# Optimization experiments

Hardware: AMD Instinct MI355X
Metric: run time of the kernel (lower is better)

## Reference

```python
import jax, jax.numpy as jnp
import numpy as np

B, LF, RATE = 2, 2048, 4
DF, DS, H = 1024, 1024, 8
D2 = DF // 2            # 512: both self (d1) and cross (d2) branch dims (equal split)
POOL_H = 2048
TS = LF // RATE         # 512 slow steps


def _p(key, shape):
    return jax.random.normal(key, shape, jnp.float32) * 0.02


def setup_inputs() -> dict:
    keys = iter(jax.random.split(jax.random.key(0), 32))
    inp = {
        "x_fast": jax.random.normal(next(keys), (B, LF, DF), jnp.float32),
        "x_slow": jax.random.normal(next(keys), (B, TS, DS), jnp.float32),
    }
    for name in ("fself", "fcross", "sself", "scross"):
        inp[f"{name}_wqkv"] = _p(next(keys), (D2, 3 * D2))
        inp[f"{name}_bqkv"] = jnp.zeros((3 * D2,), jnp.float32)
        inp[f"{name}_wo"] = _p(next(keys), (D2, D2))
        inp[f"{name}_bo"] = jnp.zeros((D2,), jnp.float32)
    inp["lift_w"] = _p(next(keys), (DS, D2))
    inp["lift_b"] = jnp.zeros((D2,), jnp.float32)
    inp["pool_w1"] = _p(next(keys), (RATE * DF, POOL_H))
    inp["pool_b1"] = jnp.zeros((POOL_H,), jnp.float32)
    inp["pool_w2"] = _p(next(keys), (POOL_H, D2))
    inp["pool_b2"] = jnp.zeros((D2,), jnp.float32)
    return inp


def _mha(q_in, k_in, v_in, wqkv, bqkv, wo, bo):
    """Standard multihead attention with fused in-proj weight [d, 3d]."""
    b, tq, d = q_in.shape
    hd = d // H
    q = q_in @ wqkv[:, :d] + bqkv[:d]
    k = k_in @ wqkv[:, d:2 * d] + bqkv[d:2 * d]
    v = v_in @ wqkv[:, 2 * d:] + bqkv[2 * d:]
    q = q.reshape(b, tq, H, hd)
    k = k.reshape(b, k_in.shape[1], H, hd)
    v = v.reshape(b, v_in.shape[1], H, hd)
    scores = jnp.einsum('bqhd,bkhd->bhqk', q, k) * np.float32(1.0 / np.sqrt(hd))
    w = jax.nn.softmax(scores, axis=-1)
    o = jnp.einsum('bhqk,bkhd->bqhd', w, v).reshape(b, tq, d)
    return o @ wo + bo


def _forward(x_fast, x_slow,
             fself_wqkv, fself_bqkv, fself_wo, fself_bo,
             fcross_wqkv, fcross_bqkv, fcross_wo, fcross_bo,
             sself_wqkv, sself_bqkv, sself_wo, sself_bo,
             scross_wqkv, scross_bqkv, scross_wo, scross_bo,
             lift_w, lift_b, pool_w1, pool_b1, pool_w2, pool_b2):
    b = x_fast.shape[0]
    # ---- fast level: lift slow -> fast timescale (ffn applied before repeat)
    y = jnp.repeat(x_slow @ lift_w + lift_b, RATE, axis=1)          # [B, LF, D2]
    x1, x2 = x_fast[..., :D2], x_fast[..., D2:]
    z_fast = jnp.concatenate([
        _mha(x1, x1, x1, fself_wqkv, fself_bqkv, fself_wo, fself_bo),
        _mha(x2, y, y, fcross_wqkv, fcross_bqkv, fcross_wo, fcross_bo),
    ], axis=-1)
    # ---- slow level: causal block pooling of fast sequence
    blocks = x_fast.reshape(b, TS, RATE * DF)                        # LF == TS*RATE
    s = jax.nn.gelu(blocks @ pool_w1 + pool_b1) @ pool_w2 + pool_b2  # [B, TS, D2]
    # causal shift: prepend zero slow step, drop last (zero in pooled feature dim)
    s = jnp.concatenate([jnp.zeros((b, 1, D2), s.dtype), s[:, :-1]], axis=1)
    s1, s2 = x_slow[..., :D2], x_slow[..., D2:]
    z_slow = jnp.concatenate([
        _mha(s1, s1, s1, sself_wqkv, sself_bqkv, sself_wo, sself_bo),
        _mha(s2, s, s, scross_wqkv, scross_bqkv, scross_wo, scross_bo),
    ], axis=-1)
    return z_fast, z_slow


def reference(x_fast, x_slow,
              fself_wqkv, fself_bqkv, fself_wo, fself_bo,
              fcross_wqkv, fcross_bqkv, fcross_wo, fcross_bo,
              sself_wqkv, sself_bqkv, sself_wo, sself_bo,
              scross_wqkv, scross_bqkv, scross_wo, scross_bo,
              lift_w, lift_b, pool_w1, pool_b1, pool_w2, pool_b2):
    return _forward(x_fast, x_slow,
                    fself_wqkv, fself_bqkv, fself_wo, fself_bo,
                    fcross_wqkv, fcross_bqkv, fcross_wo, fcross_bo,
                    sself_wqkv, sself_bqkv, sself_wo, sself_bo,
                    scross_wqkv, scross_bqkv, scross_wo, scross_bo,
                    lift_w, lift_b, pool_w1, pool_b1, pool_w2, pool_b2)
```

## Files before the change

kernel.cpp:

```cpp
#include <hip/hip_runtime.h>
#include <hip/hip_bf16.h>


typedef __attribute__((ext_vector_type(8))) short bf16x8;
typedef __attribute__((ext_vector_type(4))) float f32x4;
typedef unsigned short u16;
typedef unsigned int u32;

__device__ inline u16 f2bf(float f) {
    __hip_bfloat16 h = __float2bfloat16(f);
    return *reinterpret_cast<u16*>(&h);
}
__device__ inline u32 pack2(float a, float b) {
    return (u32)f2bf(a) | ((u32)f2bf(b) << 16);
}
__device__ inline float bf2f(u16 h) {
    u32 x = ((u32)h) << 16; float f;
    __builtin_memcpy(&f, &x, 4);
    return f;
}

#define LDT 72

struct GDesc {
    const void* A; const u16* Bt; const float* bias;
    void* out0; u16* aux0; u16* aux1;
    int lda, ldb, ldc, K, ntx, mode, rshift, aflag, tile_end, pad;
};
struct GPack { int n; int pad[3]; GDesc d[8]; };

template <int TMT>
__global__ __launch_bounds__(256)
void gemm_multi(GPack pk)
{
    constexpr int TM = TMT * 16;
    constexpr int W = TMT / 2;
    __shared__ u16 As[TM * LDT];
    __shared__ u16 Bs[TM * LDT];

    int bid = blockIdx.x;
    int di = 0;
    while (bid >= pk.d[di].tile_end) ++di;
    const GDesc g = pk.d[di];
    const int base = di ? pk.d[di - 1].tile_end : 0;
    const int local = bid - base;
    const int ty = local / g.ntx, tx = local - ty * g.ntx;
    const int row0 = ty * TM, col0 = tx * TM;

    const int t = threadIdx.x;
    const int wave = t >> 6, lane = t & 63;
    const int l15 = lane & 15, quad = lane >> 4;
    const int wm = (wave >> 1) * W * 16, wn = (wave & 1) * W * 16;
    const int sr = t >> 3, sc = t & 7;

    f32x4 acc[W][W];
#pragma unroll
    for (int i = 0; i < W; ++i)
#pragma unroll
        for (int j = 0; j < W; ++j) {
            acc[i][j][0] = 0.f; acc[i][j][1] = 0.f;
            acc[i][j][2] = 0.f; acc[i][j][3] = 0.f;
        }

    for (int k0 = 0; k0 < g.K; k0 += 64) {
        __syncthreads();
        if (g.aflag) {
            const float* Af = (const float*)g.A;
#pragma unroll
            for (int i = 0; i < TM / 32; ++i) {
                int r = sr + 32 * i;
                const float* p = Af + (long long)(row0 + r) * g.lda + k0 + sc * 8;
                float4 a = *(const float4*)p;
                float4 b = *(const float4*)(p + 4);
                uint4 u;
                u.x = pack2(a.x, a.y); u.y = pack2(a.z, a.w);
                u.z = pack2(b.x, b.y); u.w = pack2(b.z, b.w);
                *(uint4*)(As + r * LDT + sc * 8) = u;
            }
        } else {
            const u16* Ab = (const u16*)g.A;
#pragma unroll
            for (int i = 0; i < TM / 32; ++i) {
                int r = sr + 32 * i;
                *(uint4*)(As + r * LDT + sc * 8) =
                    *(const uint4*)(Ab + (long long)(row0 + r) * g.lda + k0 + sc * 8);
            }
        }
#pragma unroll
        for (int i = 0; i < TM / 32; ++i) {
            int r = sr + 32 * i;
            *(uint4*)(Bs + r * LDT + sc * 8) =
                *(const uint4*)(g.Bt + (long long)(col0 + r) * g.ldb + k0 + sc * 8);
        }
        __syncthreads();
#pragma unroll
        for (int kc = 0; kc < 2; ++kc) {
            bf16x8 af[W], bfr[W];
#pragma unroll
            for (int i = 0; i < W; ++i) {
                af[i]  = *(const bf16x8*)(As + (wm + i * 16 + l15) * LDT + kc * 32 + quad * 8);
                bfr[i] = *(const bf16x8*)(Bs + (wn + i * 16 + l15) * LDT + kc * 32 + quad * 8);
            }
#pragma unroll
            for (int i = 0; i < W; ++i)
#pragma unroll
                for (int j = 0; j < W; ++j)
                    acc[i][j] = __builtin_amdgcn_mfma_f32_16x16x32_bf16(af[i], bfr[j], acc[i][j], 0, 0, 0);
        }
    }

    const int rmask = (1 << g.rshift) - 1;
#pragma unroll
    for (int i = 0; i < W; ++i)
#pragma unroll
        for (int j = 0; j < W; ++j)
#pragma unroll
            for (int r = 0; r < 4; ++r) {
                int m = row0 + wm + i * 16 + quad * 4 + r;
                int n = col0 + wn + j * 16 + l15;
                float v = acc[i][j][r];
                if (g.mode != 5) v += g.bias[n];
                if (g.mode == 0) {
                    ((float*)g.out0)[(long long)m * g.ldc + n] = v;
                } else if (g.mode == 1 || g.mode == 5) {
                    ((u16*)g.out0)[(long long)m * g.ldc + n] = f2bf(v);
                } else if (g.mode == 3) {
                    u16 h = f2bf(v);
                    if (n < 512) ((u16*)g.out0)[(long long)m * 512 + n] = h;
                    else if (n < 1024) g.aux0[(long long)m * 512 + (n - 512)] = h;
                    else {
                        int d = n - 1024;
                        int bb = m >> g.rshift, rr = m & rmask;
                        g.aux1[((long long)((bb * 8 + (d >> 6)) * 64 + (d & 63)) << g.rshift) + rr] = h;
                    }
                } else if (g.mode == 4) {
                    u16 h = f2bf(v);
                    if (n < 512) ((u16*)g.out0)[(long long)m * 512 + n] = h;
                    else {
                        int d = n - 512;
                        int bb = m >> g.rshift, rr = m & rmask;
                        g.aux1[((long long)((bb * 8 + (d >> 6)) * 64 + (d & 63)) << g.rshift) + rr] = h;
                    }
                } else {
                    int t9 = m & 511;
                    if (t9 != 511) ((u16*)g.out0)[(long long)(m + 1) * g.ldc + n] = f2bf(v);
                    if (t9 == 0)  ((u16*)g.out0)[(long long)m * g.ldc + n] = 0;
                }
            }
}

#define ALD 72

struct ADesc { const u16* Q; const u16* K; const u16* Vt; u16* O; int Rq, nk, tile_end, pad; };
struct APack { int n; int pad[3]; ADesc d[4]; };

__global__ __launch_bounds__(256)
void attn_multi(APack pk, float prescale)
{
    __shared__ u16 Qs[64 * ALD];
    __shared__ u16 Ks[64 * ALD];
    __shared__ u16 Vts[64 * ALD];
    __shared__ u16 Ps[4][16 * ALD];

    int bid = blockIdx.x;
    int di = 0;
    while (bid >= pk.d[di].tile_end) ++di;
    const ADesc g = pk.d[di];
    const int base = di ? pk.d[di - 1].tile_end : 0;
    const int local = bid - base;

    const int t = threadIdx.x;
    const int wave = t >> 6, lane = t & 63;
    const int l15 = lane & 15, quad = lane >> 4;
    const int bh = local & 15, b = bh >> 3, h = bh & 7;
    const int q0 = (local >> 4) * 64;
    const int nk = g.nk;

    const u16* Qbase = g.Q + ((long long)(b * g.Rq + q0) << 9) + h * 64;
    const u16* Kbase = g.K + ((long long)(b * nk) << 9) + h * 64;
    const u16* Vtbase = g.Vt + (long long)bh * 64 * nk;

#pragma unroll
    for (int i = 0; i < 2; ++i) {
        int idx = t + i * 256;
        int r = idx >> 3, u4 = idx & 7;
        *(uint4*)(Qs + r * ALD + u4 * 8) = *(const uint4*)(Qbase + ((long long)r << 9) + u4 * 8);
    }
    __syncthreads();

    bf16x8 qf[2];
    qf[0] = *(const bf16x8*)(Qs + (wave * 16 + l15) * ALD + quad * 8);
    qf[1] = *(const bf16x8*)(Qs + (wave * 16 + l15) * ALD + 32 + quad * 8);

    f32x4 Oacc[4];
#pragma unroll
    for (int nt = 0; nt < 4; ++nt) { Oacc[nt][0] = 0.f; Oacc[nt][1] = 0.f; Oacc[nt][2] = 0.f; Oacc[nt][3] = 0.f; }
    float lr[4] = {0.f, 0.f, 0.f, 0.f};

    u16* Pw = &Ps[wave][0];

    for (int kt = 0; kt < nk; kt += 64) {
        __syncthreads();
#pragma unroll
        for (int i = 0; i < 2; ++i) {
            int idx = t + i * 256;
            int r = idx >> 3, u4 = idx & 7;
            *(uint4*)(Ks + r * ALD + u4 * 8) =
                *(const uint4*)(Kbase + ((long long)(kt + r) << 9) + u4 * 8);
            *(uint4*)(Vts + r * ALD + u4 * 8) =
                *(const uint4*)(Vtbase + (long long)r * nk + kt + u4 * 8);
        }
        __syncthreads();

#pragma unroll
        for (int k16 = 0; k16 < 4; ++k16) {
            f32x4 s;
            s[0] = 0.f; s[1] = 0.f; s[2] = 0.f; s[3] = 0.f;
            bf16x8 kf0 = *(const bf16x8*)(Ks + (k16 * 16 + l15) * ALD + quad * 8);
            bf16x8 kf1 = *(const bf16x8*)(Ks + (k16 * 16 + l15) * ALD + 32 + quad * 8);
            s = __builtin_amdgcn_mfma_f32_16x16x32_bf16(qf[0], kf0, s, 0, 0, 0);
            s = __builtin_amdgcn_mfma_f32_16x16x32_bf16(qf[1], kf1, s, 0, 0, 0);
#pragma unroll
            for (int r = 0; r < 4; ++r) {
                float p = exp2f(s[r] * prescale);
                lr[r] += p;
                Pw[(quad * 4 + r) * ALD + k16 * 16 + l15] = f2bf(p);
            }
        }

        bf16x8 pf0 = *(const bf16x8*)(Pw + l15 * ALD + quad * 8);
        bf16x8 pf1 = *(const bf16x8*)(Pw + l15 * ALD + 32 + quad * 8);
#pragma unroll
        for (int nt = 0; nt < 4; ++nt) {
            bf16x8 vf0 = *(const bf16x8*)(Vts + (nt * 16 + l15) * ALD + quad * 8);
            bf16x8 vf1 = *(const bf16x8*)(Vts + (nt * 16 + l15) * ALD + 32 + quad * 8);
            Oacc[nt] = __builtin_amdgcn_mfma_f32_16x16x32_bf16(pf0, vf0, Oacc[nt], 0, 0, 0);
            Oacc[nt] = __builtin_amdgcn_mfma_f32_16x16x32_bf16(pf1, vf1, Oacc[nt], 0, 0, 0);
        }
    }

    float inv[4];
#pragma unroll
    for (int r = 0; r < 4; ++r) {
        float s = lr[r];
#pragma unroll
        for (int off = 1; off < 16; off <<= 1) s += __shfl_xor(s, off);
        inv[r] = 1.f / s;
    }

    u16* Ob = g.O + ((long long)(b * g.Rq + q0 + wave * 16 + quad * 4) << 9) + h * 64;
#pragma unroll
    for (int nt = 0; nt < 4; ++nt)
#pragma unroll
        for (int r = 0; r < 4; ++r)
            Ob[(long long)r * 512 + nt * 16 + l15] = f2bf(Oacc[nt][r] * inv[r]);
}

struct WDesc { const float* src; u16* dst; int ldn, K, tx_, tile_end; };
struct WPack { int n; int pad[3]; WDesc d[6]; };

__global__ __launch_bounds__(256)
void wt_multi(WPack pk)
{
    __shared__ float T[64][68];
    int bid = blockIdx.x;
    int di = 0;
    while (bid >= pk.d[di].tile_end) ++di;
    const WDesc g = pk.d[di];
    const int base = di ? pk.d[di - 1].tile_end : 0;
    const int local = bid - base;
    const int k0 = (local % g.tx_) * 64;
    const int n0 = (local / g.tx_) * 64;
    const int t = threadIdx.x;
#pragma unroll
    for (int i = 0; i < 4; ++i) {
        int idx = t + i * 256;
        int r = idx >> 4, c4 = idx & 15;
        float4 v = *(const float4*)(g.src + (long long)(k0 + r) * g.ldn + n0 + c4 * 4);
        T[r][c4 * 4 + 0] = v.x; T[r][c4 * 4 + 1] = v.y;
        T[r][c4 * 4 + 2] = v.z; T[r][c4 * 4 + 3] = v.w;
    }
    __syncthreads();
#pragma unroll
    for (int i = 0; i < 4; ++i) {
        int idx = t + i * 256;
        int rn = idx >> 4, k4 = idx & 15;
        uint2 u;
        u.x = pack2(T[k4 * 4 + 0][rn], T[k4 * 4 + 1][rn]);
        u.y = pack2(T[k4 * 4 + 2][rn], T[k4 * 4 + 3][rn]);
        *(uint2*)(g.dst + (long long)(n0 + rn) * g.K + k0 + k4 * 4) = u;
    }
}

__global__ __launch_bounds__(256)
void gelu_sum(const u16* __restrict__ p0, const u16* __restrict__ p1,
              const float* __restrict__ bias, u16* __restrict__ out)
{
    int i8 = (blockIdx.x * 256 + threadIdx.x) * 8;
    uint4 a = *(const uint4*)(p0 + i8);
    uint4 b = *(const uint4*)(p1 + i8);
    int n = i8 & 2047;
    float4 bi0 = *(const float4*)(bias + n);
    float4 bi1 = *(const float4*)(bias + n + 4);
    float bb[8] = {bi0.x, bi0.y, bi0.z, bi0.w, bi1.x, bi1.y, bi1.z, bi1.w};
    u32 aw[4] = {a.x, a.y, a.z, a.w};
    u32 bw[4] = {b.x, b.y, b.z, b.w};
    u32 ow[4];
#pragma unroll
    for (int k = 0; k < 4; ++k) {
        float v0 = bf2f((u16)(aw[k] & 0xffff)) + bf2f((u16)(bw[k] & 0xffff)) + bb[2 * k];
        float v1 = bf2f((u16)(aw[k] >> 16)) + bf2f((u16)(bw[k] >> 16)) + bb[2 * k + 1];
        float x3 = v0 * v0 * v0;
        v0 = 0.5f * v0 * (1.f + tanhf(0.7978845608028654f * (v0 + 0.044715f * x3)));
        x3 = v1 * v1 * v1;
        v1 = 0.5f * v1 * (1.f + tanhf(0.7978845608028654f * (v1 + 0.044715f * x3)));
        ow[k] = pack2(v0, v1);
    }
    uint4 o; o.x = ow[0]; o.y = ow[1]; o.z = ow[2]; o.w = ow[3];
    *(uint4*)(out + i8) = o;
}

extern "C" void kernel_launch(void* const* d_in, const int* in_sizes, int n_in,
                              void* d_out, int out_size, void* d_ws, size_t ws_size,
                              hipStream_t stream)
{
    const float* x_fast      = (const float*)d_in[0];
    const float* x_slow      = (const float*)d_in[1];
    const float* fself_wqkv  = (const float*)d_in[2];
    const float* fself_bqkv  = (const float*)d_in[3];
    const float* fself_wo    = (const float*)d_in[4];
    const float* fself_bo    = (const float*)d_in[5];
    const float* fcross_wqkv = (const float*)d_in[6];
    const float* fcross_bqkv = (const float*)d_in[7];
    const float* fcross_wo   = (const float*)d_in[8];
    const float* fcross_bo   = (const float*)d_in[9];
    const float* sself_wqkv  = (const float*)d_in[10];
    const float* sself_bqkv  = (const float*)d_in[11];
    const float* sself_wo    = (const float*)d_in[12];
    const float* sself_bo    = (const float*)d_in[13];
    const float* scross_wqkv = (const float*)d_in[14];
    const float* scross_bqkv = (const float*)d_in[15];
    const float* scross_wo   = (const float*)d_in[16];
    const float* scross_bo   = (const float*)d_in[17];
    const float* lift_w      = (const float*)d_in[18];
    const float* lift_b      = (const float*)d_in[19];
    const float* pool_w1     = (const float*)d_in[20];
    const float* pool_b1     = (const float*)d_in[21];
    const float* pool_w2     = (const float*)d_in[22];
    const float* pool_b2     = (const float*)d_in[23];

    float* out = (float*)d_out;
    float* zf = out;
    float* zs = out + 2LL * 2048 * 1024;

    float* ws = (float*)d_ws;
    u16* wqkvT_f  = (u16*)(ws + 0);
    u16* wqkvT_c  = (u16*)(ws + 393216);
    u16* wqkvT_s  = (u16*)(ws + 786432);
    u16* wqkvT_sc = (u16*)(ws + 1179648);
    u16* liftT    = (u16*)(ws + 1572864);
    u16* pw1T     = (u16*)(ws + 1835008);
    u16* q1   = (u16*)(ws + 6029312);
    u16* k1   = (u16*)(ws + 7077888);
    u16* vt1  = (u16*)(ws + 8126464);
    u16* q2   = (u16*)(ws + 9175040);
    u16* qs   = (u16*)(ws + 10223616);
    u16* ks   = (u16*)(ws + 10485760);
    u16* vts  = (u16*)(ws + 10747904);
    u16* qcs  = (u16*)(ws + 11010048);
    u16* ybuf = (u16*)(ws + 11272192);
    u16* p0   = (u16*)(ws + 11534336);
    u16* p1   = (u16*)(ws + 12582912);
    u16* pw2T = (u16*)(ws + 13631488);
    u16* woT_f  = (u16*)(ws + 11534336);
    u16* woT_c  = (u16*)(ws + 11665408);
    u16* woT_s  = (u16*)(ws + 11796480);
    u16* woT_sc = (u16*)(ws + 11927552);
    u16* hbuf   = (u16*)(ws + 1835008);
    u16* k2     = (u16*)(ws + 12582912);
    u16* vt2    = (u16*)(ws + 12845056);
    u16* sbufS  = (u16*)(ws + 13107200);
    u16* kcs    = (u16*)(ws + 2883584);
    u16* vtcs   = (u16*)(ws + 3145728);
    u16* fo1    = (u16*)(ws + 3407872);
    u16* fo2    = (u16*)(ws + 4456448);
    u16* so1    = (u16*)(ws + 5505024);
    u16* so2    = (u16*)(ws + 5767168);

    {
        WPack p; p.n = 6;
        int te = 0, i = 0;
        auto add = [&](const float* s, u16* d, int ldn, int K, int N) {
            te += (K / 64) * (N / 64);
            p.d[i++] = WDesc{s, d, ldn, K, K / 64, te};
        };
        add(pool_w1, pw1T, 2048, 4096, 2048);
        add(fself_wqkv, wqkvT_f, 1536, 512, 1536);
        add(fcross_wqkv, wqkvT_c, 1536, 512, 1536);
        add(sself_wqkv, wqkvT_s, 1536, 512, 1536);
        add(scross_wqkv, wqkvT_sc, 1536, 512, 1536);
        add(lift_w, liftT, 512, 1024, 512);
        hipLaunchKernelGGL(wt_multi, dim3(te), dim3(256), 0, stream, p);
    }

    auto gl = [&](GPack& p, int i, const void* A, int lda, int aflag,
                  const u16* Bt, int ldb, const float* bias,
                  void* out0, int ldc, int M, int N, int K, int mode,
                  u16* aux0, u16* aux1, int rshift, int TM, int& te) {
        te += (M / TM) * (N / TM);
        p.d[i] = GDesc{A, Bt, bias, out0, aux0, aux1,
                       lda, ldb, ldc, K, N / TM, mode, rshift, aflag, te, 0};
    };

    {
        GPack p; p.n = 7; int te = 0;
        gl(p, 0, x_fast, 4096, 1, pw1T, 4096, pool_b1, p0, 2048,
           1024, 2048, 2048, 5, 0, 0, 0, 128, te);
        gl(p, 1, x_fast + 2048, 4096, 1, pw1T + 2048, 4096, pool_b1, p1, 2048,
           1024, 2048, 2048, 5, 0, 0, 0, 128, te);
        gl(p, 2, x_fast, 1024, 1, wqkvT_f, 512, fself_bqkv, q1, 512,
           4096, 1536, 512, 3, k1, vt1, 11, 128, te);
        gl(p, 3, x_fast + 512, 1024, 1, wqkvT_c, 512, fcross_bqkv, q2, 512,
           4096, 512, 512, 1, 0, 0, 0, 128, te);
        gl(p, 4, x_slow, 1024, 1, wqkvT_s, 512, sself_bqkv, qs, 512,
           1024, 1536, 512, 3, ks, vts, 9, 128, te);
        gl(p, 5, x_slow, 1024, 1, liftT, 1024, lift_b, ybuf, 512,
           1024, 512, 1024, 1, 0, 0, 0, 128, te);
        gl(p, 6, x_slow + 512, 1024, 1, wqkvT_sc, 512, scross_bqkv, qcs, 512,
           1024, 512, 512, 1, 0, 0, 0, 128, te);
        hipLaunchKernelGGL(gemm_multi<8>, dim3(te), dim3(256), 0, stream, p);
    }

    hipLaunchKernelGGL(gelu_sum, dim3(1024), dim3(256), 0, stream, p0, p1, pool_b1, hbuf);

    {
        WPack p; p.n = 5;
        int te = 0, i = 0;
        auto add = [&](const float* s, u16* d, int ldn, int K, int N) {
            te += (K / 64) * (N / 64);
            p.d[i++] = WDesc{s, d, ldn, K, K / 64, te};
        };
        add(pool_w2, pw2T, 512, 2048, 512);
        add(fself_wo, woT_f, 512, 512, 512);
        add(fcross_wo, woT_c, 512, 512, 512);
        add(sself_wo, woT_s, 512, 512, 512);
        add(scross_wo, woT_sc, 512, 512, 512);
        hipLaunchKernelGGL(wt_multi, dim3(te), dim3(256), 0, stream, p);
    }

    {
        GPack p; p.n = 2; int te = 0;
        gl(p, 0, ybuf, 512, 0, wqkvT_c + 512 * 512, 512, fcross_bqkv + 512, k2, 512,
           1024, 1024, 512, 4, 0, vt2, 9, 64, te);
        gl(p, 1, hbuf, 2048, 0, pw2T, 2048, pool_b2, sbufS, 512,
           1024, 512, 2048, 6, 0, 0, 0, 64, te);
        hipLaunchKernelGGL(gemm_multi<4>, dim3(te), dim3(256), 0, stream, p);
    }

    {
        GPack p; p.n = 1; int te = 0;
        gl(p, 0, sbufS, 512, 0, wqkvT_sc + 512 * 512, 512, scross_bqkv + 512, kcs, 512,
           1024, 1024, 512, 4, 0, vtcs, 9, 64, te);
        hipLaunchKernelGGL(gemm_multi<4>, dim3(te), dim3(256), 0, stream, p);
    }

    {
        APack p; p.n = 4;
        int te = 0, i = 0;
        auto add = [&](const u16* Q, const u16* K, const u16* Vt, u16* O, int Rq, int nk) {
            te += (Rq / 64) * 16;
            p.d[i++] = ADesc{Q, K, Vt, O, Rq, nk, te, 0};
        };
        add(q1, k1, vt1, fo1, 2048, 2048);
        add(q2, k2, vt2, fo2, 2048, 512);
        add(qs, ks, vts, so1, 512, 512);
        add(qcs, kcs, vtcs, so2, 512, 512);
        hipLaunchKernelGGL(attn_multi, dim3(te), dim3(256), 0, stream, p,
                           0.125f * 1.4426950408889634f);
    }

    {
        GPack p; p.n = 4; int te = 0;
        gl(p, 0, fo1, 512, 0, woT_f, 512, fself_bo, zf, 1024,
           4096, 512, 512, 0, 0, 0, 0, 128, te);
        gl(p, 1, fo2, 512, 0, woT_c, 512, fcross_bo, zf + 512, 1024,
           4096, 512, 512, 0, 0, 0, 0, 128, te);
        gl(p, 2, so1, 512, 0, woT_s, 512, sself_bo, zs, 1024,
           1024, 512, 512, 0, 0, 0, 0, 128, te);
        gl(p, 3, so2, 512, 0, woT_sc, 512, scross_bo, zs + 512, 1024,
           1024, 512, 512, 0, 0, 0, 0, 128, te);
        hipLaunchKernelGGL(gemm_multi<8>, dim3(te), dim3(256), 0, stream, p);
    }
}
```

Baseline: 377.7 us.

## Pre-convert inputs to bf16, use direct global-to-LDS loads, fuse GELU into pool GEMM

Adds a conversion kernel that turns x_fast and x_slow into bf16 once, so every GEMM reads bf16 A operands and no longer converts fp32 inside the tile loop. GEMM and attention tiles are now staged with global_load_lds 16-byte direct-to-LDS loads into unpadded 64-wide tiles. The split-K pool GEMM with a separate gelu_sum pass becomes a single K=4096 GEMM with GELU in its epilogue. All weight transposes are merged into one launch and workspace buffers are remapped, some of them into the output buffer. Unpadded LDS rows risk bank conflicts on the MFMA fragment reads, and the full-K pool GEMM has fewer parallel tiles.

```diff
diff --git a/kernel.cpp b/kernel.cpp
--- a/kernel.cpp
+++ b/kernel.cpp
@@ -14,18 +14,16 @@
 __device__ inline u32 pack2(float a, float b) {
     return (u32)f2bf(a) | ((u32)f2bf(b) << 16);
 }
-__device__ inline float bf2f(u16 h) {
-    u32 x = ((u32)h) << 16; float f;
-    __builtin_memcpy(&f, &x, 4);
-    return f;
-}
-
-#define LDT 72
+__device__ inline void gld16(const u16* g, u16* l) {
+    __builtin_amdgcn_global_load_lds(
+        (const __attribute__((address_space(1))) void*)(g),
+        (__attribute__((address_space(3))) void*)(l), 16, 0, 0);
+}
 
 struct GDesc {
-    const void* A; const u16* Bt; const float* bias;
+    const u16* A; const u16* Bt; const float* bias;
     void* out0; u16* aux0; u16* aux1;
-    int lda, ldb, ldc, K, ntx, mode, rshift, aflag, tile_end, pad;
+    int lda, ldb, ldc, K, ntx, mode, rshift, tile_end;
 };
 struct GPack { int n; int pad[3]; GDesc d[8]; };
 
@@ -35,8 +33,8 @@
 {
     constexpr int TM = TMT * 16;
     constexpr int W = TMT / 2;
-    __shared__ u16 As[TM * LDT];
-    __shared__ u16 Bs[TM * LDT];
+    __shared__ u16 As[TM * 64];
+    __shared__ u16 Bs[TM * 64];
 
     int bid = blockIdx.x;
     int di = 0;
@@ -51,7 +49,11 @@
     const int wave = t >> 6, lane = t & 63;
     const int l15 = lane & 15, quad = lane >> 4;
     const int wm = (wave >> 1) * W * 16, wn = (wave & 1) * W * 16;
-    const int sr = t >> 3, sc = t & 7;
+
+    const int srow = wave * 8 + (lane >> 3);
+    const int scol = (lane & 7) * 8;
+    const u16* Ag = g.A + (long long)(row0 + srow) * g.lda + scol;
+    const u16* Bg = g.Bt + (long long)(col0 + srow) * g.ldb + scol;
 
     f32x4 acc[W][W];
 #pragma unroll
@@ -64,33 +66,10 @@
 
     for (int k0 = 0; k0 < g.K; k0 += 64) {
         __syncthreads();
-        if (g.aflag) {
-            const float* Af = (const float*)g.A;
-#pragma unroll
-            for (int i = 0; i < TM / 32; ++i) {
-                int r = sr + 32 * i;
-                const float* p = Af + (long long)(row0 + r) * g.lda + k0 + sc * 8;
-                float4 a = *(const float4*)p;
-                float4 b = *(const float4*)(p + 4);
-                uint4 u;
-                u.x = pack2(a.x, a.y); u.y = pack2(a.z, a.w);
-                u.z = pack2(b.x, b.y); u.w = pack2(b.z, b.w);
-                *(uint4*)(As + r * LDT + sc * 8) = u;
-            }
-        } else {
-            const u16* Ab = (const u16*)g.A;
-#pragma unroll
-            for (int i = 0; i < TM / 32; ++i) {
-                int r = sr + 32 * i;
-                *(uint4*)(As + r * LDT + sc * 8) =
-                    *(const uint4*)(Ab + (long long)(row0 + r) * g.lda + k0 + sc * 8);
-            }
-        }
-#pragma unroll
-        for (int i = 0; i < TM / 32; ++i) {
-            int r = sr + 32 * i;
-            *(uint4*)(Bs + r * LDT + sc * 8) =
-                *(const uint4*)(g.Bt + (long long)(col0 + r) * g.ldb + k0 + sc * 8);
+#pragma unroll
+        for (int r = 0; r < TM / 32; ++r) {
+            gld16(Ag + (long long)r * 32 * g.lda + k0, As + r * 2048 + wave * 512);
+            gld16(Bg + (long long)r * 32 * g.ldb + k0, Bs + r * 2048 + wave * 512);
         }
         __syncthreads();
 #pragma unroll
@@ -98,8 +77,8 @@
             bf16x8 af[W], bfr[W];
 #pragma unroll
             for (int i = 0; i < W; ++i) {
-                af[i]  = *(const bf16x8*)(As + (wm + i * 16 + l15) * LDT + kc * 32 + quad * 8);
-                bfr[i] = *(const bf16x8*)(Bs + (wn + i * 16 + l15) * LDT + kc * 32 + quad * 8);
+                af[i]  = *(const bf16x8*)(As + (wm + i * 16 + l15) * 64 + kc * 32 + quad * 8);
+                bfr[i] = *(const bf16x8*)(Bs + (wn + i * 16 + l15) * 64 + kc * 32 + quad * 8);
             }
 #pragma unroll
             for (int i = 0; i < W; ++i)
@@ -118,11 +97,14 @@
             for (int r = 0; r < 4; ++r) {
                 int m = row0 + wm + i * 16 + quad * 4 + r;
                 int n = col0 + wn + j * 16 + l15;
-                float v = acc[i][j][r];
-                if (g.mode != 5) v += g.bias[n];
+                float v = acc[i][j][r] + g.bias[n];
                 if (g.mode == 0) {
                     ((float*)g.out0)[(long long)m * g.ldc + n] = v;
-                } else if (g.mode == 1 || g.mode == 5) {
+                } else if (g.mode == 1) {
+                    ((u16*)g.out0)[(long long)m * g.ldc + n] = f2bf(v);
+                } else if (g.mode == 2) {
+                    float x3 = v * v * v;
+                    v = 0.5f * v * (1.f + tanhf(0.7978845608028654f * (v + 0.044715f * x3)));
                     ((u16*)g.out0)[(long long)m * g.ldc + n] = f2bf(v);
                 } else if (g.mode == 3) {
                     u16 h = f2bf(v);
@@ -157,9 +139,9 @@
 __global__ __launch_bounds__(256)
 void attn_multi(APack pk, float prescale)
 {
-    __shared__ u16 Qs[64 * ALD];
-    __shared__ u16 Ks[64 * ALD];
-    __shared__ u16 Vts[64 * ALD];
+    __shared__ u16 Qs[64 * 64];
+    __shared__ u16 Ks[64 * 64];
+    __shared__ u16 Vts[64 * 64];
     __shared__ u16 Ps[4][16 * ALD];
 
     int bid = blockIdx.x;
@@ -176,21 +158,21 @@
     const int q0 = (local >> 4) * 64;
     const int nk = g.nk;
 
-    const u16* Qbase = g.Q + ((long long)(b * g.Rq + q0) << 9) + h * 64;
-    const u16* Kbase = g.K + ((long long)(b * nk) << 9) + h * 64;
-    const u16* Vtbase = g.Vt + (long long)bh * 64 * nk;
-
-#pragma unroll
-    for (int i = 0; i < 2; ++i) {
-        int idx = t + i * 256;
-        int r = idx >> 3, u4 = idx & 7;
-        *(uint4*)(Qs + r * ALD + u4 * 8) = *(const uint4*)(Qbase + ((long long)r << 9) + u4 * 8);
-    }
+    const int srow = wave * 8 + (lane >> 3);
+    const int scol = (lane & 7) * 8;
+
+    const u16* Qg = g.Q + ((long long)(b * g.Rq + q0 + srow) << 9) + h * 64 + scol;
+    const u16* Kg = g.K + ((long long)(b * nk + srow) << 9) + h * 64 + scol;
+    const u16* Vg = g.Vt + (long long)bh * 64 * nk + (long long)srow * nk + scol;
+
+#pragma unroll
+    for (int r = 0; r < 2; ++r)
+        gld16(Qg + ((long long)r * 32 << 9), Qs + r * 2048 + wave * 512);
     __syncthreads();
 
     bf16x8 qf[2];
-    qf[0] = *(const bf16x8*)(Qs + (wave * 16 + l15) * ALD + quad * 8);
-    qf[1] = *(const bf16x8*)(Qs + (wave * 16 + l15) * ALD + 32 + quad * 8);
+    qf[0] = *(const bf16x8*)(Qs + (wave * 16 + l15) * 64 + quad * 8);
+    qf[1] = *(const bf16x8*)(Qs + (wave * 16 + l15) * 64 + 32 + quad * 8);
 
     f32x4 Oacc[4];
 #pragma unroll
@@ -202,13 +184,9 @@
     for (int kt = 0; kt < nk; kt += 64) {
         __syncthreads();
 #pragma unroll
-        for (int i = 0; i < 2; ++i) {
-            int idx = t + i * 256;
-            int r = idx >> 3, u4 = idx & 7;
-            *(uint4*)(Ks + r * ALD + u4 * 8) =
-                *(const uint4*)(Kbase + ((long long)(kt + r) << 9) + u4 * 8);
-            *(uint4*)(Vts + r * ALD + u4 * 8) =
-                *(const uint4*)(Vtbase + (long long)r * nk + kt + u4 * 8);
+        for (int r = 0; r < 2; ++r) {
+            gld16(Kg + ((long long)(kt + r * 32) << 9), Ks + r * 2048 + wave * 512);
+            gld16(Vg + (long long)r * 32 * nk + kt, Vts + r * 2048 + wave * 512);
         }
         __syncthreads();
 
@@ -216,8 +194,8 @@
         for (int k16 = 0; k16 < 4; ++k16) {
             f32x4 s;
             s[0] = 0.f; s[1] = 0.f; s[2] = 0.f; s[3] = 0.f;
-            bf16x8 kf0 = *(const bf16x8*)(Ks + (k16 * 16 + l15) * ALD + quad * 8);
-            bf16x8 kf1 = *(const bf16x8*)(Ks + (k16 * 16 + l15) * ALD + 32 + quad * 8);
+            bf16x8 kf0 = *(const bf16x8*)(Ks + (k16 * 16 + l15) * 64 + quad * 8);
+            bf16x8 kf1 = *(const bf16x8*)(Ks + (k16 * 16 + l15) * 64 + 32 + quad * 8);
             s = __builtin_amdgcn_mfma_f32_16x16x32_bf16(qf[0], kf0, s, 0, 0, 0);
             s = __builtin_amdgcn_mfma_f32_16x16x32_bf16(qf[1], kf1, s, 0, 0, 0);
 #pragma unroll
@@ -232,8 +210,8 @@
         bf16x8 pf1 = *(const bf16x8*)(Pw + l15 * ALD + 32 + quad * 8);
 #pragma unroll
         for (int nt = 0; nt < 4; ++nt) {
-            bf16x8 vf0 = *(const bf16x8*)(Vts + (nt * 16 + l15) * ALD + quad * 8);
-            bf16x8 vf1 = *(const bf16x8*)(Vts + (nt * 16 + l15) * ALD + 32 + quad * 8);
+            bf16x8 vf0 = *(const bf16x8*)(Vts + (nt * 16 + l15) * 64 + quad * 8);
+            bf16x8 vf1 = *(const bf16x8*)(Vts + (nt * 16 + l15) * 64 + 32 + quad * 8);
             Oacc[nt] = __builtin_amdgcn_mfma_f32_16x16x32_bf16(pf0, vf0, Oacc[nt], 0, 0, 0);
             Oacc[nt] = __builtin_amdgcn_mfma_f32_16x16x32_bf16(pf1, vf1, Oacc[nt], 0, 0, 0);
         }
@@ -257,7 +235,7 @@
 }
 
 struct WDesc { const float* src; u16* dst; int ldn, K, tx_, tile_end; };
-struct WPack { int n; int pad[3]; WDesc d[6]; };
+struct WPack { int n; int pad[3]; WDesc d[12]; };
 
 __global__ __launch_bounds__(256)
 void wt_multi(WPack pk)
@@ -293,31 +271,19 @@
 }
 
 __global__ __launch_bounds__(256)
-void gelu_sum(const u16* __restrict__ p0, const u16* __restrict__ p1,
-              const float* __restrict__ bias, u16* __restrict__ out)
+void c_cvt2(const float* __restrict__ a, u16* __restrict__ da, int na8,
+            const float* __restrict__ b, u16* __restrict__ db)
 {
-    int i8 = (blockIdx.x * 256 + threadIdx.x) * 8;
-    uint4 a = *(const uint4*)(p0 + i8);
-    uint4 b = *(const uint4*)(p1 + i8);
-    int n = i8 & 2047;
-    float4 bi0 = *(const float4*)(bias + n);
-    float4 bi1 = *(const float4*)(bias + n + 4);
-    float bb[8] = {bi0.x, bi0.y, bi0.z, bi0.w, bi1.x, bi1.y, bi1.z, bi1.w};
-    u32 aw[4] = {a.x, a.y, a.z, a.w};
-    u32 bw[4] = {b.x, b.y, b.z, b.w};
-    u32 ow[4];
-#pragma unroll
-    for (int k = 0; k < 4; ++k) {
-        float v0 = bf2f((u16)(aw[k] & 0xffff)) + bf2f((u16)(bw[k] & 0xffff)) + bb[2 * k];
-        float v1 = bf2f((u16)(aw[k] >> 16)) + bf2f((u16)(bw[k] >> 16)) + bb[2 * k + 1];
-        float x3 = v0 * v0 * v0;
-        v0 = 0.5f * v0 * (1.f + tanhf(0.7978845608028654f * (v0 + 0.044715f * x3)));
-        x3 = v1 * v1 * v1;
-        v1 = 0.5f * v1 * (1.f + tanhf(0.7978845608028654f * (v1 + 0.044715f * x3)));
-        ow[k] = pack2(v0, v1);
-    }
-    uint4 o; o.x = ow[0]; o.y = ow[1]; o.z = ow[2]; o.w = ow[3];
-    *(uint4*)(out + i8) = o;
+    int i = blockIdx.x * 256 + threadIdx.x;
+    const float* s; u16* d;
+    if (i < na8) { s = a + (long long)i * 8; d = da + (long long)i * 8; }
+    else { s = b + (long long)(i - na8) * 8; d = db + (long long)(i - na8) * 8; }
+    float4 x = *(const float4*)s;
+    float4 y = *(const float4*)(s + 4);
+    uint4 u;
+    u.x = pack2(x.x, x.y); u.y = pack2(x.z, x.w);
+    u.z = pack2(y.x, y.y); u.w = pack2(y.z, y.w);
+    *(uint4*)d = u;
 }
 
 extern "C" void kernel_launch(void* const* d_in, const int* in_sizes, int n_in,
@@ -354,41 +320,44 @@
     float* zs = out + 2LL * 2048 * 1024;
 
     float* ws = (float*)d_ws;
-    u16* wqkvT_f  = (u16*)(ws + 0);
-    u16* wqkvT_c  = (u16*)(ws + 393216);
-    u16* wqkvT_s  = (u16*)(ws + 786432);
-    u16* wqkvT_sc = (u16*)(ws + 1179648);
-    u16* liftT    = (u16*)(ws + 1572864);
-    u16* pw1T     = (u16*)(ws + 1835008);
-    u16* q1   = (u16*)(ws + 6029312);
-    u16* k1   = (u16*)(ws + 7077888);
-    u16* vt1  = (u16*)(ws + 8126464);
-    u16* q2   = (u16*)(ws + 9175040);
-    u16* qs   = (u16*)(ws + 10223616);
-    u16* ks   = (u16*)(ws + 10485760);
-    u16* vts  = (u16*)(ws + 10747904);
-    u16* qcs  = (u16*)(ws + 11010048);
-    u16* ybuf = (u16*)(ws + 11272192);
-    u16* p0   = (u16*)(ws + 11534336);
-    u16* p1   = (u16*)(ws + 12582912);
-    u16* pw2T = (u16*)(ws + 13631488);
-    u16* woT_f  = (u16*)(ws + 11534336);
-    u16* woT_c  = (u16*)(ws + 11665408);
-    u16* woT_s  = (u16*)(ws + 11796480);
-    u16* woT_sc = (u16*)(ws + 11927552);
-    u16* hbuf   = (u16*)(ws + 1835008);
-    u16* k2     = (u16*)(ws + 12582912);
-    u16* vt2    = (u16*)(ws + 12845056);
-    u16* sbufS  = (u16*)(ws + 13107200);
-    u16* kcs    = (u16*)(ws + 2883584);
-    u16* vtcs   = (u16*)(ws + 3145728);
-    u16* fo1    = (u16*)(ws + 3407872);
-    u16* fo2    = (u16*)(ws + 4456448);
-    u16* so1    = (u16*)(ws + 5505024);
-    u16* so2    = (u16*)(ws + 5767168);
-
-    {
-        WPack p; p.n = 6;
+    u16* pw1T     = (u16*)(ws + 0);
+    u16* wqkvT_f  = (u16*)(ws + 4194304);
+    u16* wqkvT_c  = (u16*)(ws + 4587520);
+    u16* wqkvT_s  = (u16*)(ws + 4980736);
+    u16* wqkvT_sc = (u16*)(ws + 5373952);
+    u16* liftT    = (u16*)(ws + 5767168);
+    u16* pw2T     = (u16*)(ws + 6029312);
+    u16* woT_f    = (u16*)(ws + 6553600);
+    u16* woT_c    = (u16*)(ws + 6684672);
+    u16* woT_s    = (u16*)(ws + 6815744);
+    u16* woT_sc   = (u16*)(ws + 6946816);
+    u16* xfb      = (u16*)(ws + 7077888);
+    u16* xsb      = (u16*)(ws + 9175040);
+    u16* q1       = (u16*)(ws + 9699328);
+    u16* k1       = (u16*)(ws + 10747904);
+    u16* vt1      = (u16*)(ws + 11796480);
+    u16* qs       = (u16*)(ws + 12845056);
+    u16* ks       = (u16*)(ws + 13107200);
+    u16* vts      = (u16*)(ws + 13369344);
+    u16* qcs      = (u16*)(ws + 13631488);
+    u16* k2    = (u16*)(ws + 0);
+    u16* vt2   = (u16*)(ws + 262144);
+    u16* sbufS = (u16*)(ws + 524288);
+    u16* kcs   = (u16*)(ws + 786432);
+    u16* vtcs  = (u16*)(ws + 1048576);
+    u16* fo1   = (u16*)(ws + 1310720);
+    u16* fo2   = (u16*)(ws + 2359296);
+    u16* so1   = (u16*)(ws + 3407872);
+    u16* so2   = (u16*)(ws + 3670016);
+    u16* q2   = (u16*)(out + 0);
+    u16* ybuf = (u16*)(out + 1048576);
+    u16* hbuf = (u16*)(out + 1310720);
+
+    hipLaunchKernelGGL(c_cvt2, dim3(2560), dim3(256), 0, stream,
+                       x_fast, xfb, 524288, x_slow, xsb);
+
+    {
+        WPack p; p.n = 11;
         int te = 0, i = 0;
         auto add = [&](const float* s, u16* d, int ldn, int K, int N) {
             te += (K / 64) * (N / 64);
@@ -400,46 +369,6 @@
         add(sself_wqkv, wqkvT_s, 1536, 512, 1536);
         add(scross_wqkv, wqkvT_sc, 1536, 512, 1536);
         add(lift_w, liftT, 512, 1024, 512);
-        hipLaunchKernelGGL(wt_multi, dim3(te), dim3(256), 0, stream, p);
-    }
-
-    auto gl = [&](GPack& p, int i, const void* A, int lda, int aflag,
-                  const u16* Bt, int ldb, const float* bias,
-                  void* out0, int ldc, int M, int N, int K, int mode,
-                  u16* aux0, u16* aux1, int rshift, int TM, int& te) {
-        te += (M / TM) * (N / TM);
-        p.d[i] = GDesc{A, Bt, bias, out0, aux0, aux1,
-                       lda, ldb, ldc, K, N / TM, mode, rshift, aflag, te, 0};
-    };
-
-    {
-        GPack p; p.n = 7; int te = 0;
-        gl(p, 0, x_fast, 4096, 1, pw1T, 4096, pool_b1, p0, 2048,
-           1024, 2048, 2048, 5, 0, 0, 0, 128, te);
-        gl(p, 1, x_fast + 2048, 4096, 1, pw1T + 2048, 4096, pool_b1, p1, 2048,
-           1024, 2048, 2048, 5, 0, 0, 0, 128, te);
-        gl(p, 2, x_fast, 1024, 1, wqkvT_f, 512, fself_bqkv, q1, 512,
-           4096, 1536, 512, 3, k1, vt1, 11, 128, te);
-        gl(p, 3, x_fast + 512, 1024, 1, wqkvT_c, 512, fcross_bqkv, q2, 512,
-           4096, 512, 512, 1, 0, 0, 0, 128, te);
-        gl(p, 4, x_slow, 1024, 1, wqkvT_s, 512, sself_bqkv, qs, 512,
-           1024, 1536, 512, 3, ks, vts, 9, 128, te);
-        gl(p, 5, x_slow, 1024, 1, liftT, 1024, lift_b, ybuf, 512,
-           1024, 512, 1024, 1, 0, 0, 0, 128, te);
-        gl(p, 6, x_slow + 512, 1024, 1, wqkvT_sc, 512, scross_bqkv, qcs, 512,
-           1024, 512, 512, 1, 0, 0, 0, 128, te);
-        hipLaunchKernelGGL(gemm_multi<8>, dim3(te), dim3(256), 0, stream, p);
-    }
-
-    hipLaunchKernelGGL(gelu_sum, dim3(1024), dim3(256), 0, stream, p0, p1, pool_b1, hbuf);
-
-    {
-        WPack p; p.n = 5;
-        int te = 0, i = 0;
-        auto add = [&](const float* s, u16* d, int ldn, int K, int N) {
-            te += (K / 64) * (N / 64);
-            p.d[i++] = WDesc{s, d, ldn, K, K / 64, te};
-        };
         add(pool_w2, pw2T, 512, 2048, 512);
         add(fself_wo, woT_f, 512, 512, 512);
         add(fcross_wo, woT_c, 512, 512, 512);
@@ -448,18 +377,44 @@
         hipLaunchKernelGGL(wt_multi, dim3(te), dim3(256), 0, stream, p);
     }
 
+    auto gl = [&](GPack& p, int i, const u16* A, int lda,
+                  const u16* Bt, int ldb, const float* bias,
+                  void* out0, int ldc, int M, int N, int K, int mode,
+                  u16* aux0, u16* aux1, int rshift, int TM, int& te) {
+        te += (M / TM) * (N / TM);
+        p.d[i] = GDesc{A, Bt, bias, out0, aux0, aux1,
+                       lda, ldb, ldc, K, N / TM, mode, rshift, te};
+    };
+
+    {
+        GPack p; p.n = 6; int te = 0;
+        gl(p, 0, xfb, 4096, pw1T, 4096, pool_b1, hbuf, 2048,
+           1024, 2048, 4096, 2, 0, 0, 0, 128, te);
+        gl(p, 1, xfb, 1024, wqkvT_f, 512, fself_bqkv, q1, 512,
+           4096, 1536, 512, 3, k1, vt1, 11, 128, te);
+        gl(p, 2, xfb + 512, 1024, wqkvT_c, 512, fcross_bqkv, q2, 512,
+           4096, 512, 512, 1, 0, 0, 0, 128, te);
+        gl(p, 3, xsb, 1024, wqkvT_s, 512, sself_bqkv, qs, 512,
+           1024, 1536, 512, 3, ks, vts, 9, 128, te);
+        gl(p, 4, xsb, 1024, liftT, 1024, lift_b, ybuf, 512,
+           1024, 512, 1024, 1, 0, 0, 0, 128, te);
+        gl(p, 5, xsb + 512, 1024, wqkvT_sc, 512, scross_bqkv, qcs, 512,
+           1024, 512, 512, 1, 0, 0, 0, 128, te);
+        hipLaunchKernelGGL(gemm_multi<8>, dim3(te), dim3(256), 0, stream, p);
+    }
+
     {
         GPack p; p.n = 2; int te = 0;
-        gl(p, 0, ybuf, 512, 0, wqkvT_c + 512 * 512, 512, fcross_bqkv + 512, k2, 512,
+        gl(p, 0, ybuf, 512, wqkvT_c + 512 * 512, 512, fcross_bqkv + 512, k2, 512,
            1024, 1024, 512, 4, 0, vt2, 9, 64, te);
-        gl(p, 1, hbuf, 2048, 0, pw2T, 2048, pool_b2, sbufS, 512,
+        gl(p, 1, hbuf, 2048, pw2T, 2048, pool_b2, sbufS, 512,
            1024, 512, 2048, 6, 0, 0, 0, 64, te);
         hipLaunchKernelGGL(gemm_multi<4>, dim3(te), dim3(256), 0, stream, p);
     }
 
     {
         GPack p; p.n = 1; int te = 0;
-        gl(p, 0, sbufS, 512, 0, wqkvT_sc + 512 * 512, 512, scross_bqkv + 512, kcs, 512,
+        gl(p, 0, sbufS, 512, wqkvT_sc + 512 * 512, 512, scross_bqkv + 512, kcs, 512,
            1024, 1024, 512, 4, 0, vtcs, 9, 64, te);
         hipLaunchKernelGGL(gemm_multi<4>, dim3(te), dim3(256), 0, stream, p);
     }
@@ -481,13 +436,13 @@
 
     {
         GPack p; p.n = 4; int te = 0;
-        gl(p, 0, fo1, 512, 0, woT_f, 512, fself_bo, zf, 1024,
+        gl(p, 0, fo1, 512, woT_f, 512, fself_bo, zf, 1024,
            4096, 512, 512, 0, 0, 0, 0, 128, te);
-        gl(p, 1, fo2, 512, 0, woT_c, 512, fcross_bo, zf + 512, 1024,
+        gl(p, 1, fo2, 512, woT_c, 512, fcross_bo, zf + 512, 1024,
            4096, 512, 512, 0, 0, 0, 0, 128, te);
-        gl(p, 2, so1, 512, 0, woT_s, 512, sself_bo, zs, 1024,
+        gl(p, 2, so1, 512, woT_s, 512, sself_bo, zs, 1024,
            1024, 512, 512, 0, 0, 0, 0, 128, te);
-        gl(p, 3, so2, 512, 0, woT_sc, 512, scross_bo, zs + 512, 1024,
+        gl(p, 3, so2, 512, woT_sc, 512, scross_bo, zs + 512, 1024,
            1024, 512, 512, 0, 0, 0, 0, 128, te);
         hipLaunchKernelGGL(gemm_multi<8>, dim3(te), dim3(256), 0, stream, p);
     }
```

Result: slower. 390.9 us (+3.5%).
